# Kernel tuning notes

Measured on AMD Instinct MI355X. Metric: run time of the kernel, lower is better.

## Reference

```python
import jax, jax.numpy as jnp
import numpy as np

N_NODES = 100000
N_EDGES = 600000
HIDDEN = 128
BN_EPS = 1e-5


def setup_inputs() -> dict:
    key = jax.random.key(0)
    k_x, k_e, k_w, k_b, k_g = jax.random.split(key, 5)
    x = jax.random.normal(k_x, (N_NODES, HIDDEN), dtype=jnp.float32)
    edge_index = jax.random.randint(k_e, (2, N_EDGES), 0, N_NODES, dtype=jnp.int64)
    # GCNConv linear weight (no bias on the linear; bias added post-aggregation)
    scale = 1.0 / np.sqrt(HIDDEN)
    W = jax.random.uniform(k_w, (HIDDEN, HIDDEN), jnp.float32, -scale, scale)
    b = jax.random.uniform(k_b, (HIDDEN,), jnp.float32, -scale, scale)
    gamma = jnp.ones((HIDDEN,), jnp.float32)   # BatchNorm weight
    beta = jnp.zeros((HIDDEN,), jnp.float32)   # BatchNorm bias
    return {"x": x, "edge_index": edge_index, "W": W, "b": b, "gamma": gamma, "beta": beta}


def reference(x, edge_index, W, b, gamma, beta):
    N = x.shape[0]
    # ReLU then GCNConv linear transform: [N, D]
    h = jnp.matmul(jax.nn.relu(x), W)
    # Add self-loops (PyG GCNConv default)
    loops = jnp.arange(N, dtype=edge_index.dtype)
    row = jnp.concatenate([edge_index[0], loops])  # source nodes
    col = jnp.concatenate([edge_index[1], loops])  # target nodes
    # Symmetric normalization deg^{-1/2} with unit edge weights
    ones = jnp.ones(row.shape[0], dtype=h.dtype)
    deg = jax.ops.segment_sum(ones, col, num_segments=N)
    dinv = jnp.where(deg > 0, jax.lax.rsqrt(deg), 0.0)
    norm = dinv[row] * dinv[col]  # [E+N]
    # Gather -> scale -> scatter-add aggregation, then conv bias
    agg = jax.ops.segment_sum(norm[:, None] * h[row], col, num_segments=N)
    out = agg + b
    # BatchNorm1d (training mode: batch stats, biased variance)
    mean = jnp.mean(out, axis=0)
    var = jnp.var(out, axis=0)
    return gamma * (out - mean) * jax.lax.rsqrt(var + BN_EPS) + beta
```

## Files before the change

kernel.cpp:

```cpp
#include <hip/hip_runtime.h>

#define D 128
#define CAP 32
#define BN_EPS 1e-5f

typedef float floatx4 __attribute__((ext_vector_type(4)));
typedef __bf16 bf16x8 __attribute__((ext_vector_type(8)));

__device__ inline unsigned short f2bf(float f) {
    unsigned u; __builtin_memcpy(&u, &f, 4);
    unsigned r = (u + 0x7FFFu + ((u >> 16) & 1u)) >> 16;
    return (unsigned short)r;
}
__device__ inline float bflo(unsigned v) { unsigned x = v << 16; float f; __builtin_memcpy(&f, &x, 4); return f; }
__device__ inline float bfhi(unsigned v) { unsigned x = v & 0xFFFF0000u; float f; __builtin_memcpy(&f, &x, 4); return f; }

__global__ void setup_k(const unsigned* __restrict__ e, int* __restrict__ flag,
                        int* __restrict__ cursor, float* __restrict__ sums,
                        float* __restrict__ sumsq, const float* __restrict__ W,
                        unsigned short* __restrict__ Wt, int n_nodes) {
    int i = blockIdx.x * blockDim.x + threadIdx.x;
    if (i < n_nodes) cursor[i] = 0;
    if (i < D) { sums[i] = 0.f; sumsq[i] = 0.f; }
    if (i < D * D) {
        int n = i >> 7, k = i & 127;
        Wt[n * D + k] = f2bf(W[k * D + n]);
    }
    if (i == 0) {
        unsigned acc = 0;
        for (int k = 0; k < 64; ++k) acc |= e[2 * k + 1];
        *flag = (acc == 0u) ? 1 : 0;
    }
}

__global__ __launch_bounds__(256, 2) void gb_k(const float* __restrict__ x,
                                               const unsigned short* __restrict__ Wt,
                                               unsigned short* __restrict__ h,
                                               int n_mtiles,
                                               const void* __restrict__ ep,
                                               const int* __restrict__ flag,
                                               int* __restrict__ cursor,
                                               int* __restrict__ bucket,
                                               int n_edges) {
    int b = blockIdx.x;
    int g = b >> 3;
    int ngroups = (int)gridDim.x >> 3;
    int nbg = ngroups >> 2;

    if ((g & 3) == 3) {
        int bb = (g >> 2) * 8 + (b & 7);
        int stride = nbg * 8 * 256;
        int fl = *flag;
        for (int e = bb * 256 + (int)threadIdx.x; e < n_edges; e += stride) {
            int r, c;
            if (fl) {
                const long long* p = (const long long*)ep;
                r = (int)p[e]; c = (int)p[e + n_edges];
            } else {
                const int* p = (const int*)ep;
                r = p[e]; c = p[e + n_edges];
            }
            int pos = atomicAdd(&cursor[c], 1);
            if (pos < CAP) bucket[(size_t)c * CAP + pos] = r;
        }
        return;
    }

    int gg = (g >> 2) * 3 + (g & 3);
    int gb = gg * 8 + (b & 7);
    int lane = threadIdx.x & 63;
    int wave = gb * 4 + (threadIdx.x >> 6);
    int nw = (ngroups - nbg) * 32;
    int l15 = lane & 15;
    int quad = lane >> 4;

    bf16x8 Bf[4][8];
    for (int ks = 0; ks < 4; ++ks)
        for (int j = 0; j < 8; ++j)
            Bf[ks][j] = *(const bf16x8*)(Wt + (size_t)(j * 16 + l15) * D + ks * 32 + quad * 8);

    for (int mt = wave; mt < n_mtiles; mt += nw) {
        const float* xrow = x + (size_t)(mt * 16 + l15) * D + quad * 8;
        bf16x8 Af[4];
        for (int ks = 0; ks < 4; ++ks) {
            float4 a0 = *(const float4*)(xrow + ks * 32);
            float4 a1 = *(const float4*)(xrow + ks * 32 + 4);
            float av[8] = {a0.x, a0.y, a0.z, a0.w, a1.x, a1.y, a1.z, a1.w};
            union { unsigned short u[8]; bf16x8 v; } tmp;
            for (int jj = 0; jj < 8; ++jj) tmp.u[jj] = f2bf(fmaxf(av[jj], 0.0f));
            Af[ks] = tmp.v;
        }
        floatx4 acc[8];
        for (int j = 0; j < 8; ++j) acc[j] = (floatx4){0.f, 0.f, 0.f, 0.f};
        for (int ks = 0; ks < 4; ++ks)
            for (int j = 0; j < 8; ++j)
                acc[j] = __builtin_amdgcn_mfma_f32_16x16x32_bf16(Af[ks], Bf[ks][j], acc[j], 0, 0, 0);
        for (int j = 0; j < 8; ++j)
            for (int reg = 0; reg < 4; ++reg) {
                int rr = mt * 16 + quad * 4 + reg;
                int cc = j * 16 + l15;
                h[(size_t)rr * D + cc] = f2bf(acc[j][reg]);
            }
    }
}

#define PREPD(s, rr) { int r_ = ((s) < degc) ? (rr) : node;                         \
                       float cd_ = (float)cursor[r_];                                \
                       w##s = ((s) < degc) ? rsqrtf(1.0f + cd_) : 0.0f;              \
                       hv##s = hp[(unsigned)r_ * 64u + lane]; }
#define ACC(s) { ax += w##s * bflo(hv##s); ay += w##s * bfhi(hv##s); }

__global__ __launch_bounds__(256) void agg_k(const unsigned short* __restrict__ h,
                                             const int* __restrict__ bucket,
                                             const int* __restrict__ cursor,
                                             unsigned* __restrict__ aggb,
                                             float* __restrict__ partials,
                                             int n_nodes) {
    __shared__ float red[256];
    int lane = threadIdx.x & 63;
    int wib = threadIdx.x >> 6;
    int nw = gridDim.x * 4;
    const unsigned* hp = (const unsigned*)h;
    float s0 = 0.f, s1 = 0.f, q0 = 0.f, q1 = 0.f;

    for (int node = blockIdx.x * 4 + wib; node < n_nodes; node += nw) {
        int deg = cursor[node];
        int degc = deg < CAP ? deg : CAP;
        float dc = rsqrtf(1.0f + (float)deg);

        unsigned v = hp[(unsigned)node * 64u + lane];
        float ax = dc * bflo(v), ay = dc * bfhi(v);
        const int* bk = bucket + (size_t)node * CAP;

        float w0=0,w1=0,w2=0,w3=0,w4=0,w5=0,w6=0,w7=0;
        unsigned hv0=0,hv1=0,hv2=0,hv3=0,hv4=0,hv5=0,hv6=0,hv7=0;

        if (degc > 0) { int4 b4 = *(const int4*)(bk);     PREPD(0,b4.x) PREPD(1,b4.y) PREPD(2,b4.z) PREPD(3,b4.w) }
        if (degc > 4) { int4 b4 = *(const int4*)(bk + 4); PREPD(4,b4.x) PREPD(5,b4.y) PREPD(6,b4.z) PREPD(7,b4.w) }

        if (degc <= 8) {
            ACC(0) ACC(1) ACC(2) ACC(3) ACC(4) ACC(5) ACC(6) ACC(7)
        } else {
            float w8=0,w9=0,w10=0,w11=0,w12=0,w13=0,w14=0,w15=0;
            unsigned hv8=0,hv9=0,hv10=0,hv11=0,hv12=0,hv13=0,hv14=0,hv15=0;
            { int4 b4 = *(const int4*)(bk + 8); PREPD(8,b4.x) PREPD(9,b4.y) PREPD(10,b4.z) PREPD(11,b4.w) }
            if (degc > 12) { int4 b4 = *(const int4*)(bk + 12); PREPD(12,b4.x) PREPD(13,b4.y) PREPD(14,b4.z) PREPD(15,b4.w) }
            ACC(0)  ACC(1)  ACC(2)  ACC(3)  ACC(4)  ACC(5)  ACC(6)  ACC(7)
            ACC(8)  ACC(9)  ACC(10) ACC(11) ACC(12) ACC(13) ACC(14) ACC(15)
            for (int e = 16; e < degc; ++e) {
                int r = bk[e];
                float dr = rsqrtf(1.0f + (float)cursor[r]);
                unsigned hh = hp[(unsigned)r * 64u + lane];
                ax += dr * bflo(hh); ay += dr * bfhi(hh);
            }
        }

        float ox = dc * ax, oy = dc * ay;
        unsigned pk = ((unsigned)f2bf(oy) << 16) | (unsigned)f2bf(ox);
        __builtin_nontemporal_store(pk, &aggb[(unsigned)node * 64u + lane]);
        s0 += ox; s1 += oy; q0 += ox * ox; q1 += oy * oy;
    }

    float* pb = partials + (size_t)blockIdx.x * 256;
    red[threadIdx.x] = s0; __syncthreads();
    if (wib == 0) pb[2 * lane]       = red[lane] + red[64 + lane] + red[128 + lane] + red[192 + lane];
    __syncthreads(); red[threadIdx.x] = s1; __syncthreads();
    if (wib == 0) pb[2 * lane + 1]   = red[lane] + red[64 + lane] + red[128 + lane] + red[192 + lane];
    __syncthreads(); red[threadIdx.x] = q0; __syncthreads();
    if (wib == 0) pb[128 + 2 * lane] = red[lane] + red[64 + lane] + red[128 + lane] + red[192 + lane];
    __syncthreads(); red[threadIdx.x] = q1; __syncthreads();
    if (wib == 0) pb[129 + 2 * lane] = red[lane] + red[64 + lane] + red[128 + lane] + red[192 + lane];
}

__global__ __launch_bounds__(256) void stats2_k(const float* __restrict__ partials,
                                                float* __restrict__ sums, float* __restrict__ sumsq,
                                                int nblk) {
    int tid = threadIdx.x;
    int per = nblk / gridDim.x;
    int b0 = blockIdx.x * per;
    float acc = 0.f;
    for (int bb = b0; bb < b0 + per; ++bb) acc += partials[(size_t)bb * 256 + tid];
    if (tid < 128) atomicAdd(&sums[tid], acc);
    else           atomicAdd(&sumsq[tid - 128], acc);
}

__global__ __launch_bounds__(256) void final_k(const unsigned* __restrict__ aggb,
                                               const float* __restrict__ sums, const float* __restrict__ sumsq,
                                               const float* __restrict__ gamma, const float* __restrict__ beta,
                                               float* __restrict__ out, int total4, float inv_n) {
    int i = blockIdx.x * blockDim.x + threadIdx.x;
    if (i >= total4) return;
    int idx = i * 4;
    int f = idx & (D - 1);
    float4 sm = *(const float4*)(sums + f);
    float4 sq = *(const float4*)(sumsq + f);
    float4 g  = *(const float4*)(gamma + f);
    float4 bt = *(const float4*)(beta + f);
    uint2 p = *(const uint2*)(aggb + i * 2);

    float m0 = sm.x * inv_n, m1 = sm.y * inv_n, m2 = sm.z * inv_n, m3 = sm.w * inv_n;
    float sc0 = g.x * rsqrtf(sq.x * inv_n - m0 * m0 + BN_EPS);
    float sc1 = g.y * rsqrtf(sq.y * inv_n - m1 * m1 + BN_EPS);
    float sc2 = g.z * rsqrtf(sq.z * inv_n - m2 * m2 + BN_EPS);
    float sc3 = g.w * rsqrtf(sq.w * inv_n - m3 * m3 + BN_EPS);
    float4 o;
    o.x = fmaf(bflo(p.x), sc0, bt.x - m0 * sc0);
    o.y = fmaf(bfhi(p.x), sc1, bt.y - m1 * sc1);
    o.z = fmaf(bflo(p.y), sc2, bt.z - m2 * sc2);
    o.w = fmaf(bfhi(p.y), sc3, bt.w - m3 * sc3);
    *(float4*)(out + idx) = o;
}

extern "C" void kernel_launch(void* const* d_in, const int* in_sizes, int n_in,
                              void* d_out, int out_size, void* d_ws, size_t ws_size,
                              hipStream_t stream) {
    const float* x     = (const float*)d_in[0];
    const void*  edges = d_in[1];
    const float* W     = (const float*)d_in[2];
    const float* gamma = (const float*)d_in[4];
    const float* beta  = (const float*)d_in[5];
    float* out = (float*)d_out;

    int N = in_sizes[0] / D;
    int E = in_sizes[1] / 2;

    char* ws = (char*)d_ws;
    size_t off = 0;
    auto alloc = [&](size_t bytes) { void* p = ws + off; off += (bytes + 255) & ~(size_t)255; return p; };
    unsigned short* h  = (unsigned short*)alloc((size_t)N * D * 2);
    unsigned* aggb     = (unsigned*)alloc((size_t)N * D * 2);
    int* bucket        = (int*)alloc((size_t)N * CAP * 4);
    int* cursor        = (int*)alloc((size_t)N * 4);
    unsigned short* Wt = (unsigned short*)alloc((size_t)D * D * 2);
    float* partials    = (float*)alloc((size_t)2048 * 256 * 4);
    float* sums        = (float*)alloc(512);
    float* sumsq       = (float*)alloc(512);
    int* flag          = (int*)alloc(16);

    int nblk = (N + 255) / 256;
    int n_mtiles = N / 16;

    setup_k<<<nblk, 256, 0, stream>>>((const unsigned*)edges, flag, cursor, sums, sumsq, W, Wt, N);
    gb_k<<<2080, 256, 0, stream>>>(x, Wt, h, n_mtiles, edges, flag, cursor, bucket, E);
    agg_k<<<2048, 256, 0, stream>>>(h, bucket, cursor, aggb, partials, N);
    stats2_k<<<32, 256, 0, stream>>>(partials, sums, sumsq, 2048);
    final_k<<<(N * D / 4 + 255) / 256, 256, 0, stream>>>(aggb, sums, sumsq, gamma, beta, out, N * D / 4, 1.0f / (float)N);
}
```

Before: 260.8 us.

## Split stats out of aggregation and fuse stats+normalize into cooperative kernel

```diff
diff --git a/kernel.cpp b/kernel.cpp
--- a/kernel.cpp
+++ b/kernel.cpp
@@ -1,4 +1,7 @@
 #include <hip/hip_runtime.h>
+#include <hip/hip_cooperative_groups.h>
+
+namespace cg = cooperative_groups;
 
 #define D 128
 #define CAP 32
@@ -104,9 +107,9 @@
     }
 }
 
-#define PREPD(s, rr) { int r_ = ((s) < degc) ? (rr) : node;                         \
-                       float cd_ = (float)cursor[r_];                                \
-                       w##s = ((s) < degc) ? rsqrtf(1.0f + cd_) : 0.0f;              \
+#define PREPD(s, rr) { int r_ = ((s) < degc) ? (rr) : node;                        \
+                       int d_ = cursor[r_];                                         \
+                       w##s = ((s) < degc) ? rsqrtf(1.0f + (float)d_) : 0.0f;       \
                        hv##s = hp[(unsigned)r_ * 64u + lane]; }
 #define ACC(s) { ax += w##s * bflo(hv##s); ay += w##s * bfhi(hv##s); }
 
@@ -114,101 +117,132 @@
                                              const int* __restrict__ bucket,
                                              const int* __restrict__ cursor,
                                              unsigned* __restrict__ aggb,
-                                             float* __restrict__ partials,
                                              int n_nodes) {
+    int lane = threadIdx.x & 63;
+    int node = blockIdx.x * 4 + (threadIdx.x >> 6);
+    if (node >= n_nodes) return;
+    const unsigned* hp = (const unsigned*)h;
+
+    int deg = cursor[node];
+    int degc = deg < CAP ? deg : CAP;
+    float dc = rsqrtf(1.0f + (float)deg);
+
+    unsigned v = hp[(unsigned)node * 64u + lane];
+    float ax = dc * bflo(v), ay = dc * bfhi(v);
+    const int* bk = bucket + (size_t)node * CAP;
+
+    float w0=0,w1=0,w2=0,w3=0,w4=0,w5=0,w6=0,w7=0;
+    unsigned hv0=0,hv1=0,hv2=0,hv3=0,hv4=0,hv5=0,hv6=0,hv7=0;
+
+    if (degc > 0) { int4 b = *(const int4*)(bk);     PREPD(0,b.x) PREPD(1,b.y) PREPD(2,b.z) PREPD(3,b.w) }
+    if (degc > 4) { int4 b = *(const int4*)(bk + 4); PREPD(4,b.x) PREPD(5,b.y) PREPD(6,b.z) PREPD(7,b.w) }
+
+    if (degc <= 8) {
+        ACC(0) ACC(1) ACC(2) ACC(3) ACC(4) ACC(5) ACC(6) ACC(7)
+    } else {
+        float w8=0,w9=0,w10=0,w11=0,w12=0,w13=0,w14=0,w15=0;
+        unsigned hv8=0,hv9=0,hv10=0,hv11=0,hv12=0,hv13=0,hv14=0,hv15=0;
+        { int4 b = *(const int4*)(bk + 8); PREPD(8,b.x) PREPD(9,b.y) PREPD(10,b.z) PREPD(11,b.w) }
+        if (degc > 12) { int4 b = *(const int4*)(bk + 12); PREPD(12,b.x) PREPD(13,b.y) PREPD(14,b.z) PREPD(15,b.w) }
+        ACC(0)  ACC(1)  ACC(2)  ACC(3)  ACC(4)  ACC(5)  ACC(6)  ACC(7)
+        ACC(8)  ACC(9)  ACC(10) ACC(11) ACC(12) ACC(13) ACC(14) ACC(15)
+        for (int e = 16; e < degc; ++e) {
+            int r = bk[e];
+            float dr = rsqrtf(1.0f + (float)cursor[r]);
+            unsigned hh = hp[(unsigned)r * 64u + lane];
+            ax += dr * bflo(hh); ay += dr * bfhi(hh);
+        }
+    }
+
+    float ox = dc * ax, oy = dc * ay;
+    aggb[(unsigned)node * 64u + lane] = ((unsigned)f2bf(oy) << 16) | (unsigned)f2bf(ox);
+}
+
+__global__ __launch_bounds__(256) void sf_k(const unsigned* __restrict__ aggb,
+                                            float* __restrict__ partials,
+                                            float* __restrict__ sums, float* __restrict__ sumsq,
+                                            const float* __restrict__ gamma, const float* __restrict__ beta,
+                                            float* __restrict__ out, float* __restrict__ ss,
+                                            int N, float inv_n) {
+    cg::grid_group grid = cg::this_grid();
     __shared__ float red[256];
     int lane = threadIdx.x & 63;
     int wib = threadIdx.x >> 6;
-    int nw = gridDim.x * 4;
-    const unsigned* hp = (const unsigned*)h;
-    float s0 = 0.f, s1 = 0.f, q0 = 0.f, q1 = 0.f;
-
-    for (int node = blockIdx.x * 4 + wib; node < n_nodes; node += nw) {
-        int deg = cursor[node];
-        int degc = deg < CAP ? deg : CAP;
-        float dc = rsqrtf(1.0f + (float)deg);
-
-        unsigned v = hp[(unsigned)node * 64u + lane];
-        float ax = dc * bflo(v), ay = dc * bfhi(v);
-        const int* bk = bucket + (size_t)node * CAP;
-
-        float w0=0,w1=0,w2=0,w3=0,w4=0,w5=0,w6=0,w7=0;
-        unsigned hv0=0,hv1=0,hv2=0,hv3=0,hv4=0,hv5=0,hv6=0,hv7=0;
-
-        if (degc > 0) { int4 b4 = *(const int4*)(bk);     PREPD(0,b4.x) PREPD(1,b4.y) PREPD(2,b4.z) PREPD(3,b4.w) }
-        if (degc > 4) { int4 b4 = *(const int4*)(bk + 4); PREPD(4,b4.x) PREPD(5,b4.y) PREPD(6,b4.z) PREPD(7,b4.w) }
-
-        if (degc <= 8) {
-            ACC(0) ACC(1) ACC(2) ACC(3) ACC(4) ACC(5) ACC(6) ACC(7)
-        } else {
-            float w8=0,w9=0,w10=0,w11=0,w12=0,w13=0,w14=0,w15=0;
-            unsigned hv8=0,hv9=0,hv10=0,hv11=0,hv12=0,hv13=0,hv14=0,hv15=0;
-            { int4 b4 = *(const int4*)(bk + 8); PREPD(8,b4.x) PREPD(9,b4.y) PREPD(10,b4.z) PREPD(11,b4.w) }
-            if (degc > 12) { int4 b4 = *(const int4*)(bk + 12); PREPD(12,b4.x) PREPD(13,b4.y) PREPD(14,b4.z) PREPD(15,b4.w) }
-            ACC(0)  ACC(1)  ACC(2)  ACC(3)  ACC(4)  ACC(5)  ACC(6)  ACC(7)
-            ACC(8)  ACC(9)  ACC(10) ACC(11) ACC(12) ACC(13) ACC(14) ACC(15)
-            for (int e = 16; e < degc; ++e) {
-                int r = bk[e];
-                float dr = rsqrtf(1.0f + (float)cursor[r]);
-                unsigned hh = hp[(unsigned)r * 64u + lane];
-                ax += dr * bflo(hh); ay += dr * bfhi(hh);
-            }
-        }
-
-        float ox = dc * ax, oy = dc * ay;
-        unsigned pk = ((unsigned)f2bf(oy) << 16) | (unsigned)f2bf(ox);
-        __builtin_nontemporal_store(pk, &aggb[(unsigned)node * 64u + lane]);
-        s0 += ox; s1 += oy; q0 += ox * ox; q1 += oy * oy;
-    }
-
-    float* pb = partials + (size_t)blockIdx.x * 256;
-    red[threadIdx.x] = s0; __syncthreads();
-    if (wib == 0) pb[2 * lane]       = red[lane] + red[64 + lane] + red[128 + lane] + red[192 + lane];
-    __syncthreads(); red[threadIdx.x] = s1; __syncthreads();
-    if (wib == 0) pb[2 * lane + 1]   = red[lane] + red[64 + lane] + red[128 + lane] + red[192 + lane];
-    __syncthreads(); red[threadIdx.x] = q0; __syncthreads();
-    if (wib == 0) pb[128 + 2 * lane] = red[lane] + red[64 + lane] + red[128 + lane] + red[192 + lane];
-    __syncthreads(); red[threadIdx.x] = q1; __syncthreads();
-    if (wib == 0) pb[129 + 2 * lane] = red[lane] + red[64 + lane] + red[128 + lane] + red[192 + lane];
-}
-
-__global__ __launch_bounds__(256) void stats2_k(const float* __restrict__ partials,
-                                                float* __restrict__ sums, float* __restrict__ sumsq,
-                                                int nblk) {
-    int tid = threadIdx.x;
-    int per = nblk / gridDim.x;
-    int b0 = blockIdx.x * per;
-    float acc = 0.f;
-    for (int bb = b0; bb < b0 + per; ++bb) acc += partials[(size_t)bb * 256 + tid];
-    if (tid < 128) atomicAdd(&sums[tid], acc);
-    else           atomicAdd(&sumsq[tid - 128], acc);
-}
-
-__global__ __launch_bounds__(256) void final_k(const unsigned* __restrict__ aggb,
-                                               const float* __restrict__ sums, const float* __restrict__ sumsq,
-                                               const float* __restrict__ gamma, const float* __restrict__ beta,
-                                               float* __restrict__ out, int total4, float inv_n) {
-    int i = blockIdx.x * blockDim.x + threadIdx.x;
-    if (i >= total4) return;
-    int idx = i * 4;
-    int f = idx & (D - 1);
-    float4 sm = *(const float4*)(sums + f);
-    float4 sq = *(const float4*)(sumsq + f);
-    float4 g  = *(const float4*)(gamma + f);
-    float4 bt = *(const float4*)(beta + f);
-    uint2 p = *(const uint2*)(aggb + i * 2);
-
-    float m0 = sm.x * inv_n, m1 = sm.y * inv_n, m2 = sm.z * inv_n, m3 = sm.w * inv_n;
-    float sc0 = g.x * rsqrtf(sq.x * inv_n - m0 * m0 + BN_EPS);
-    float sc1 = g.y * rsqrtf(sq.y * inv_n - m1 * m1 + BN_EPS);
-    float sc2 = g.z * rsqrtf(sq.z * inv_n - m2 * m2 + BN_EPS);
-    float sc3 = g.w * rsqrtf(sq.w * inv_n - m3 * m3 + BN_EPS);
-    float4 o;
-    o.x = fmaf(bflo(p.x), sc0, bt.x - m0 * sc0);
-    o.y = fmaf(bfhi(p.x), sc1, bt.y - m1 * sc1);
-    o.z = fmaf(bflo(p.y), sc2, bt.z - m2 * sc2);
-    o.w = fmaf(bfhi(p.y), sc3, bt.w - m3 * sc3);
-    *(float4*)(out + idx) = o;
+
+    {
+        int nw = (int)gridDim.x * 4;
+        float s0 = 0.f, s1 = 0.f, q0 = 0.f, q1 = 0.f;
+        int n = blockIdx.x * 4 + wib;
+        for (; n + 3 * nw < N; n += 4 * nw) {
+            unsigned p0 = aggb[(size_t)n * 64 + lane];
+            unsigned p1 = aggb[(size_t)(n + nw) * 64 + lane];
+            unsigned p2 = aggb[(size_t)(n + 2 * nw) * 64 + lane];
+            unsigned p3 = aggb[(size_t)(n + 3 * nw) * 64 + lane];
+            float a0 = bflo(p0), b0 = bfhi(p0), a1 = bflo(p1), b1 = bfhi(p1);
+            float a2 = bflo(p2), b2 = bfhi(p2), a3 = bflo(p3), b3 = bfhi(p3);
+            s0 += a0 + a1 + a2 + a3;
+            s1 += b0 + b1 + b2 + b3;
+            q0 += a0 * a0 + a1 * a1 + a2 * a2 + a3 * a3;
+            q1 += b0 * b0 + b1 * b1 + b2 * b2 + b3 * b3;
+        }
+        for (; n < N; n += nw) {
+            unsigned p = aggb[(size_t)n * 64 + lane];
+            float vx = bflo(p), vy = bfhi(p);
+            s0 += vx; s1 += vy; q0 += vx * vx; q1 += vy * vy;
+        }
+        float* pb = partials + (size_t)blockIdx.x * 256;
+        red[threadIdx.x] = s0; __syncthreads();
+        if (wib == 0) pb[2 * lane]       = red[lane] + red[64 + lane] + red[128 + lane] + red[192 + lane];
+        __syncthreads(); red[threadIdx.x] = s1; __syncthreads();
+        if (wib == 0) pb[2 * lane + 1]   = red[lane] + red[64 + lane] + red[128 + lane] + red[192 + lane];
+        __syncthreads(); red[threadIdx.x] = q0; __syncthreads();
+        if (wib == 0) pb[128 + 2 * lane] = red[lane] + red[64 + lane] + red[128 + lane] + red[192 + lane];
+        __syncthreads(); red[threadIdx.x] = q1; __syncthreads();
+        if (wib == 0) pb[129 + 2 * lane] = red[lane] + red[64 + lane] + red[128 + lane] + red[192 + lane];
+    }
+    grid.sync();
+
+    if (blockIdx.x < 32) {
+        int tid = threadIdx.x;
+        int per = (int)gridDim.x / 32;
+        int b0 = blockIdx.x * per;
+        float acc = 0.f;
+        for (int bb = b0; bb < b0 + per; ++bb) acc += partials[(size_t)bb * 256 + tid];
+        if (tid < 128) atomicAdd(&sums[tid], acc);
+        else           atomicAdd(&sumsq[tid - 128], acc);
+    }
+    grid.sync();
+
+    {
+        int t = blockIdx.x * 256 + (int)threadIdx.x;
+        if (t < 128) {
+            float m = sums[t] * inv_n;
+            float v = sumsq[t] * inv_n - m * m;
+            float sc = gamma[t] * rsqrtf(v + BN_EPS);
+            ss[t] = sc;
+            ss[128 + t] = beta[t] - m * sc;
+        }
+    }
+    grid.sync();
+
+    {
+        int total4 = N * (D / 4);
+        int t = blockIdx.x * 256 + (int)threadIdx.x;
+        int nth = (int)gridDim.x * 256;
+        for (int i = t; i < total4; i += nth) {
+            int idx = i * 4;
+            int f = idx & (D - 1);
+            float4 sc4 = *(const float4*)(ss + f);
+            float4 sh4 = *(const float4*)(ss + 128 + f);
+            uint2 p = *(const uint2*)(aggb + (size_t)i * 2);
+            float4 o;
+            o.x = fmaf(bflo(p.x), sc4.x, sh4.x);
+            o.y = fmaf(bfhi(p.x), sc4.y, sh4.y);
+            o.z = fmaf(bflo(p.y), sc4.z, sh4.z);
+            o.w = fmaf(bfhi(p.y), sc4.w, sh4.w);
+            *(float4*)(out + idx) = o;
+        }
+    }
 }
 
 extern "C" void kernel_launch(void* const* d_in, const int* in_sizes, int n_in,
@@ -235,14 +269,26 @@
     float* partials    = (float*)alloc((size_t)2048 * 256 * 4);
     float* sums        = (float*)alloc(512);
     float* sumsq       = (float*)alloc(512);
+    float* ss          = (float*)alloc(1024);
     int* flag          = (int*)alloc(16);
 
     int nblk = (N + 255) / 256;
     int n_mtiles = N / 16;
+    float inv_n = 1.0f / (float)N;
 
     setup_k<<<nblk, 256, 0, stream>>>((const unsigned*)edges, flag, cursor, sums, sumsq, W, Wt, N);
     gb_k<<<2080, 256, 0, stream>>>(x, Wt, h, n_mtiles, edges, flag, cursor, bucket, E);
-    agg_k<<<2048, 256, 0, stream>>>(h, bucket, cursor, aggb, partials, N);
-    stats2_k<<<32, 256, 0, stream>>>(partials, sums, sumsq, 2048);
-    final_k<<<(N * D / 4 + 255) / 256, 256, 0, stream>>>(aggb, sums, sumsq, gamma, beta, out, N * D / 4, 1.0f / (float)N);
-}
+    agg_k<<<(N + 3) / 4, 256, 0, stream>>>(h, bucket, cursor, aggb, N);
+
+    int maxb = 0;
+    hipOccupancyMaxActiveBlocksPerMultiprocessor(&maxb, sf_k, 256, 0);
+    if (maxb < 1) maxb = 1;
+    int sgrid = maxb * 256;
+    if (sgrid > 2048) sgrid = 2048;
+    sgrid &= ~63;
+    if (sgrid < 64) sgrid = 64;
+    void* args[] = { (void*)&aggb, (void*)&partials, (void*)&sums, (void*)&sumsq,
+                     (void*)&gamma, (void*)&beta, (void*)&out, (void*)&ss,
+                     (void*)&N, (void*)&inv_n };
+    hipLaunchCooperativeKernel((const void*)sf_k, dim3(sgrid), dim3(256), args, 0, stream);
+}
```

Result: slower. 763.2 us (+192.6%).
